# Kernel tuning notes

Hardware: AMD Instinct MI355X
Metric: run time of the kernel (lower is better)

The kernel has to match this reference:

```python
import jax, jax.numpy as jnp
import numpy as np

N = 100000   # nodes
E = 1600000  # edges
G = 256      # graphs in batch
F_IN = 64
H = 64
C = 10


def setup_inputs() -> dict:
    key = jax.random.key(0)
    ks = jax.random.split(key, 16)
    x = jax.random.normal(ks[0], (N, F_IN), dtype=jnp.float32)
    edge_index = jax.random.randint(ks[1], (2, E), 0, N, dtype=jnp.int32)
    batch = jnp.sort(jax.random.randint(ks[2], (N,), 0, G, dtype=jnp.int32))
    def lin(k, i, o):
        return jax.random.normal(k, (i, o), dtype=jnp.float32) / np.sqrt(i).astype(np.float32)
    return {
        'x': x, 'edge_index': edge_index, 'batch': batch,
        'W1': lin(ks[3], F_IN, H), 'b1': jnp.zeros((H,), jnp.float32),
        'W2': lin(ks[4], H, H),    'b2': jnp.zeros((H,), jnp.float32),
        'W3': lin(ks[5], H, H),    'b3': jnp.zeros((H,), jnp.float32),
        'fc1_w': lin(ks[6], 3 * H, H),      'fc1_b': jnp.zeros((H,), jnp.float32),
        'fc2_w': lin(ks[7], H, H // 2),     'fc2_b': jnp.zeros((H // 2,), jnp.float32),
        'fc3_w': lin(ks[8], H // 2, C),     'fc3_b': jnp.zeros((C,), jnp.float32),
    }


def _gcn_layer(h_in, W, b, src, dst, deg_inv_sqrt):
    # GCNConv: h = X W ; out = D^-1/2 (A + I) D^-1/2 h + b ; then ReLU
    h = h_in @ W
    norm = deg_inv_sqrt[src] * deg_inv_sqrt[dst]            # [E]
    agg = jax.ops.segment_sum(h[src] * norm[:, None], dst, num_segments=N)
    agg = agg + h * (deg_inv_sqrt * deg_inv_sqrt)[:, None]  # self-loop term
    return jax.nn.relu(agg + b)


def _pool(h, batch):
    # concat(mean, max, add) pooling by graph id
    s = jax.ops.segment_sum(h, batch, num_segments=G)
    cnt = jax.ops.segment_sum(jnp.ones((h.shape[0], 1), h.dtype), batch, num_segments=G)
    mean = s / jnp.maximum(cnt, 1.0)
    mx = jnp.maximum(jax.ops.segment_max(h, batch, num_segments=G), 0.0)  # h >= 0 post-ReLU
    return jnp.concatenate([mean, mx, s], axis=1)  # [G, 3H]


def reference(x, edge_index, batch, W1, b1, W2, b2, W3, b3,
              fc1_w, fc1_b, fc2_w, fc2_b, fc3_w, fc3_b):
    src, dst = edge_index[0], edge_index[1]
    # degree including self loop (edge weight 1)
    deg = jax.ops.segment_sum(jnp.ones((E,), x.dtype), dst, num_segments=N) + 1.0
    dis = jax.lax.rsqrt(deg)

    h1 = _gcn_layer(x, W1, b1, src, dst, dis)
    p1 = _pool(h1, batch)
    h2 = _gcn_layer(h1, W2, b2, src, dst, dis)
    p2 = _pool(h2, batch)
    h3 = _gcn_layer(h2, W3, b3, src, dst, dis)
    p3 = _pool(h3, batch)

    z = p1 + p2 + p3                              # [G, 3H]
    z = jax.nn.relu(z @ fc1_w + fc1_b)            # dropout inactive (eval)
    z = jax.nn.relu(z @ fc2_w + fc2_b)
    return jax.nn.log_softmax(z @ fc3_w + fc3_b, axis=-1)
```

## Files before the change

kernel.cpp:

```cpp
#include <hip/hip_runtime.h>
#include <cmath>

typedef unsigned int uint;
typedef __attribute__((ext_vector_type(8))) short short8;
typedef __attribute__((ext_vector_type(4))) float f32x4;
typedef __attribute__((ext_vector_type(4))) int i32x4;

__device__ inline float bflo(uint u) { return __uint_as_float(u << 16); }
__device__ inline float bfhi(uint u) { return __uint_as_float(u & 0xffff0000u); }
__device__ inline ushort bf1(float a) {
  uint ua = __float_as_uint(a);
  return (ushort)((ua + 0x7fffu + ((ua >> 16) & 1u)) >> 16);
}
__device__ inline uint bfpack(float a, float b) {
  uint ua = __float_as_uint(a), ub = __float_as_uint(b);
  uint ra = (ua + 0x7fffu + ((ua >> 16) & 1u)) >> 16;
  uint rb = (ub + 0x7fffu + ((ub >> 16) & 1u)) >> 16;
  return ra | (rb << 16);
}

#define SLOT_CAP 48
#define FILL_CHUNK 4096
#define BSHIFT 8
#define NPB 256
#define MAXB 512
#define BCAP 5120

__global__ __launch_bounds__(256) void part_k(const int* __restrict__ src, const int* __restrict__ dst,
                                              int* __restrict__ bcnt, long long* __restrict__ buckets,
                                              int E, int nb) {
  __shared__ int lcnt[MAXB], lbase[MAXB];
  int t = threadIdx.x;
  for (int i = t; i < nb; i += 256) lcnt[i] = 0;
  __syncthreads();
  int base = blockIdx.x * FILL_CHUNK;
  int d[16];
  #pragma unroll
  for (int i = 0; i < 16; ++i) {
    int e = base + t + i * 256;
    d[i] = (e < E) ? __builtin_nontemporal_load(dst + e) : -1;
    if (d[i] >= 0) atomicAdd(&lcnt[d[i] >> BSHIFT], 1);
  }
  __syncthreads();
  for (int i = t; i < nb; i += 256) { lbase[i] = atomicAdd(&bcnt[i], lcnt[i]); lcnt[i] = 0; }
  __syncthreads();
  #pragma unroll
  for (int i = 0; i < 16; ++i) {
    if (d[i] >= 0) {
      int e = base + t + i * 256;
      int r = d[i] >> BSHIFT;
      int rank = atomicAdd(&lcnt[r], 1);
      long long s = (long long)__builtin_nontemporal_load(src + e);
      long long packed = (s << 32) | (unsigned int)d[i];
      buckets[(size_t)r * BCAP + lbase[r] + rank] = packed;
    }
  }
}

__global__ __launch_bounds__(256) void fillB_k(const long long* __restrict__ buckets,
                                               const int* __restrict__ bcnt,
                                               int* __restrict__ cursor, int* __restrict__ csr,
                                               int nb, int N) {
  __shared__ int lcnt[NPB];
  __shared__ int rows[NPB][SLOT_CAP];
  int r = blockIdx.x;
  int t = threadIdx.x;
  if (t < NPB) lcnt[t] = 0;
  i32x4* rinit = (i32x4*)&rows[0][0];
  for (int i = t; i < NPB * SLOT_CAP / 4; i += 256) rinit[i] = (i32x4){N, N, N, N};
  __syncthreads();
  int n = bcnt[r];
  const long long* bk = buckets + (size_t)r * BCAP;
  for (int i = t; i < n; i += 256) {
    long long e = __builtin_nontemporal_load(&bk[i]);
    int dl = (int)(e & (NPB - 1));
    int s = (int)(e >> 32);
    int pos = atomicAdd(&lcnt[dl], 1);
    if (pos < SLOT_CAP) rows[dl][pos] = s;
  }
  __syncthreads();
  int base_node = r << BSHIFT;
  int nodes_here = N - base_node; if (nodes_here > NPB) nodes_here = NPB;
  if (nodes_here <= 0) return;
  int total4 = nodes_here * (SLOT_CAP / 4);
  i32x4* dstp = (i32x4*)(csr + (size_t)base_node * SLOT_CAP);
  const i32x4* srcp = (const i32x4*)&rows[0][0];
  for (int i = t; i < total4; i += 256) dstp[i] = srcp[i];
  for (int i = t; i < nodes_here; i += 256) cursor[base_node + i] = lcnt[i];
}

__global__ __launch_bounds__(256) void dis_k(const int* __restrict__ cursor, float* __restrict__ dis, int n) {
  int i = blockIdx.x * 256 + threadIdx.x;
  if (i < n) dis[i] = rsqrtf((float)cursor[i] + 1.0f);
}

__global__ __launch_bounds__(256) void bounds_k(const int* __restrict__ batch, int* __restrict__ gstart,
                                                int n, int G) {
  int i = blockIdx.x * 256 + threadIdx.x;
  if (i >= n) return;
  int b = batch[i];
  int prev = (i == 0) ? -1 : batch[i - 1];
  for (int g = prev + 1; g <= b; ++g) gstart[g] = i;
  if (i == n - 1) { for (int g = b + 1; g <= G; ++g) gstart[g] = n; }
}

__global__ __launch_bounds__(256) void xcast_k(const float* __restrict__ X, ushort* __restrict__ Y, int total4) {
  int i = blockIdx.x * 256 + threadIdx.x;
  if (i >= total4) return;
  float4 v = ((const float4*)X)[i];
  ((uint2*)Y)[i] = make_uint2(bfpack(v.x, v.y), bfpack(v.z, v.w));
}

__global__ __launch_bounds__(256) void wt_k(const float* __restrict__ W, ushort* __restrict__ WT) {
  int i = blockIdx.x * 256 + threadIdx.x;
  int c = i >> 6, k = i & 63;
  WT[i] = bf1(W[k * 64 + c]);
}

__global__ __launch_bounds__(256) void gemm_mfma_k(const ushort* __restrict__ X,
                                                   const ushort* __restrict__ WT,
                                                   const float* __restrict__ dis,
                                                   ushort* __restrict__ Y, int n) {
  int t = threadIdx.x;
  int wv = t >> 6, lane = t & 63;
  int m = lane & 15, quad = lane >> 4;
  int row = blockIdx.x * 64 + wv * 16 + m;
  int rclamp = (row < n) ? row : 0;
  const short8* arow = (const short8*)(X + (size_t)rclamp * 64);
  short8 a0 = arow[quad];
  short8 a1 = arow[quad + 4];
  f32x4 acc[4];
  #pragma unroll
  for (int ct = 0; ct < 4; ++ct) {
    const short8* wrow = (const short8*)(WT + (size_t)(ct * 16 + m) * 64);
    short8 b0 = wrow[quad];
    short8 b1 = wrow[quad + 4];
    f32x4 a = {0.f, 0.f, 0.f, 0.f};
    a = __builtin_amdgcn_mfma_f32_16x16x32_bf16(a0, b0, a, 0, 0, 0);
    a = __builtin_amdgcn_mfma_f32_16x16x32_bf16(a1, b1, a, 0, 0, 0);
    acc[ct] = a;
  }
  int orow = blockIdx.x * 64 + wv * 16 + quad * 4;
  #pragma unroll
  for (int reg = 0; reg < 4; ++reg) {
    int r = orow + reg;
    if (r < n) {
      float ds = dis[r];
      #pragma unroll
      for (int ct = 0; ct < 4; ++ct)
        Y[(size_t)r * 64 + ct * 16 + m] = bf1(acc[ct][reg] * ds);
    }
  }
}

__global__ __launch_bounds__(256) void agg_k(const ushort* __restrict__ Hs,
                                             const int* __restrict__ csr,
                                             const int* __restrict__ cnt,
                                             const float* __restrict__ dis,
                                             const float* __restrict__ bias,
                                             ushort* __restrict__ Hout, int n) {
  int wv = __builtin_amdgcn_readfirstlane((int)(threadIdx.x >> 6));
  int lane = threadIdx.x & 63;
  int node = blockIdx.x * 4 + wv;
  if (node >= n) return;
  float dn = dis[node];
  int deg = __builtin_nontemporal_load(cnt + node);
  if (deg > SLOT_CAP) deg = SLOT_CAP;
  const i32x4* rp = (const i32x4*)(csr + (size_t)node * SLOT_CAP);
  float acc = bflo((uint)Hs[(size_t)node * 64 + lane]);

  i32x4 ra0 = __builtin_nontemporal_load(rp + 0);
  i32x4 ra1 = __builtin_nontemporal_load(rp + 1);
  i32x4 ra2 = __builtin_nontemporal_load(rp + 2);
  i32x4 ra3 = __builtin_nontemporal_load(rp + 3);
  int sa[16] = {ra0.x, ra0.y, ra0.z, ra0.w,
                ra1.x, ra1.y, ra1.z, ra1.w,
                ra2.x, ra2.y, ra2.z, ra2.w,
                ra3.x, ra3.y, ra3.z, ra3.w};
  float ha[16];
  #pragma unroll
  for (int i = 0; i < 16; ++i) ha[i] = bflo((uint)Hs[(size_t)sa[i] * 64 + lane]);
  #pragma unroll
  for (int i = 0; i < 16; ++i) acc += ha[i];

  if (deg > 16) {
    i32x4 rb0 = __builtin_nontemporal_load(rp + 4);
    i32x4 rb1 = __builtin_nontemporal_load(rp + 5);
    i32x4 rb2 = __builtin_nontemporal_load(rp + 6);
    i32x4 rb3 = __builtin_nontemporal_load(rp + 7);
    int sb[16] = {rb0.x, rb0.y, rb0.z, rb0.w,
                  rb1.x, rb1.y, rb1.z, rb1.w,
                  rb2.x, rb2.y, rb2.z, rb2.w,
                  rb3.x, rb3.y, rb3.z, rb3.w};
    float hb[16];
    #pragma unroll
    for (int i = 0; i < 16; ++i) hb[i] = bflo((uint)Hs[(size_t)sb[i] * 64 + lane]);
    #pragma unroll
    for (int i = 0; i < 16; ++i) acc += hb[i];

    if (deg > 32) {
      i32x4 rc0 = __builtin_nontemporal_load(rp + 8);
      i32x4 rc1 = __builtin_nontemporal_load(rp + 9);
      i32x4 rc2 = __builtin_nontemporal_load(rp + 10);
      i32x4 rc3 = __builtin_nontemporal_load(rp + 11);
      int sc[16] = {rc0.x, rc0.y, rc0.z, rc0.w,
                    rc1.x, rc1.y, rc1.z, rc1.w,
                    rc2.x, rc2.y, rc2.z, rc2.w,
                    rc3.x, rc3.y, rc3.z, rc3.w};
      float hc[16];
      #pragma unroll
      for (int i = 0; i < 16; ++i) hc[i] = bflo((uint)Hs[(size_t)sc[i] * 64 + lane]);
      #pragma unroll
      for (int i = 0; i < 16; ++i) acc += hc[i];
    }
  }

  float v = fmaxf(fmaf(dn, acc, bias[lane]), 0.f);
  Hout[(size_t)node * 64 + lane] = bf1(v);
}

__global__ __launch_bounds__(256) void pool_k(const ushort* __restrict__ H, const int* __restrict__ gstart,
                                              float* __restrict__ z) {
  int g = blockIdx.x;
  int t = threadIdx.x;
  int lane = t & 63, w = t >> 6;
  int slot = lane >> 3, fl = lane & 7;
  int i0 = gstart[g], i1 = gstart[g + 1];
  float s[8], m[8];
  #pragma unroll
  for (int j = 0; j < 8; ++j) { s[j] = 0.f; m[j] = 0.f; }
  for (int i = i0 + w * 8 + slot; i < i1; i += 32) {
    uint4 v = ((const uint4*)(H + (size_t)i * 64))[fl];
    float f[8] = { bflo(v.x), bfhi(v.x), bflo(v.y), bfhi(v.y),
                   bflo(v.z), bfhi(v.z), bflo(v.w), bfhi(v.w) };
    #pragma unroll
    for (int j = 0; j < 8; ++j) { s[j] += f[j]; m[j] = fmaxf(m[j], f[j]); }
  }
  #pragma unroll
  for (int msk = 8; msk <= 32; msk <<= 1) {
    #pragma unroll
    for (int j = 0; j < 8; ++j) {
      s[j] += __shfl_xor(s[j], msk, 64);
      m[j] = fmaxf(m[j], __shfl_xor(m[j], msk, 64));
    }
  }
  __shared__ float ss[4][64], sm[4][64];
  if (slot == 0) {
    #pragma unroll
    for (int j = 0; j < 8; ++j) { ss[w][fl * 8 + j] = s[j]; sm[w][fl * 8 + j] = m[j]; }
  }
  __syncthreads();
  if (t < 64) {
    float S = ss[0][t] + ss[1][t] + ss[2][t] + ss[3][t];
    float M = fmaxf(fmaxf(sm[0][t], sm[1][t]), fmaxf(sm[2][t], sm[3][t]));
    float cnt = (float)(i1 - i0);
    float mean = (cnt > 0.f) ? S / cnt : 0.f;
    z[g * 192 + t]       += mean;
    z[g * 192 + 64 + t]  += M;
    z[g * 192 + 128 + t] += S;
  }
}

__global__ __launch_bounds__(64) void mlp_k(const float* __restrict__ z,
                                            const float* __restrict__ fc1w, const float* __restrict__ fc1b,
                                            const float* __restrict__ fc2w, const float* __restrict__ fc2b,
                                            const float* __restrict__ fc3w, const float* __restrict__ fc3b,
                                            float* __restrict__ out) {
  int g = blockIdx.x; int t = threadIdx.x;
  __shared__ float zr[192], a1[64], a2[32], a3[10];
  for (int i = t; i < 192; i += 64) zr[i] = z[g * 192 + i];
  __syncthreads();
  float acc = fc1b[t];
  for (int k = 0; k < 192; ++k) acc += zr[k] * fc1w[k * 64 + t];
  a1[t] = fmaxf(acc, 0.f);
  __syncthreads();
  if (t < 32) {
    float a = fc2b[t];
    #pragma unroll
    for (int k = 0; k < 64; ++k) a += a1[k] * fc2w[k * 32 + t];
    a2[t] = fmaxf(a, 0.f);
  }
  __syncthreads();
  if (t < 10) {
    float a = fc3b[t];
    #pragma unroll
    for (int k = 0; k < 32; ++k) a += a2[k] * fc3w[k * 10 + t];
    a3[t] = a;
  }
  __syncthreads();
  if (t == 0) {
    float mx = a3[0];
    for (int i = 1; i < 10; ++i) mx = fmaxf(mx, a3[i]);
    float sum = 0.f;
    for (int i = 0; i < 10; ++i) sum += expf(a3[i] - mx);
    float lse = mx + logf(sum);
    for (int i = 0; i < 10; ++i) out[g * 10 + i] = a3[i] - lse;
  }
}

extern "C" void kernel_launch(void* const* d_in, const int* in_sizes, int n_in,
                              void* d_out, int out_size, void* d_ws, size_t ws_size,
                              hipStream_t stream) {
  const float* x    = (const float*)d_in[0];
  const int*   ei   = (const int*)  d_in[1];
  const int*   batch= (const int*)  d_in[2];
  const float* W1   = (const float*)d_in[3];
  const float* b1   = (const float*)d_in[4];
  const float* W2   = (const float*)d_in[5];
  const float* b2   = (const float*)d_in[6];
  const float* W3   = (const float*)d_in[7];
  const float* b3   = (const float*)d_in[8];
  const float* fc1w = (const float*)d_in[9];
  const float* fc1b = (const float*)d_in[10];
  const float* fc2w = (const float*)d_in[11];
  const float* fc2b = (const float*)d_in[12];
  const float* fc3w = (const float*)d_in[13];
  const float* fc3b = (const float*)d_in[14];
  float* out = (float*)d_out;

  const int N = in_sizes[0] / 64;
  const int E = in_sizes[1] / 2;
  const int G = out_size / 10;
  const int* src = ei;
  const int* dst = ei + E;
  const int nb = (N + NPB - 1) >> BSHIFT;

  char* p = (char*)d_ws;
  auto alloc = [&](size_t bytes) -> void* {
    void* r = (void*)p; p += (bytes + 255) & ~(size_t)255; return r;
  };
  int*       cursor  = (int*)      alloc((size_t)N * 4);
  int*       bcnt    = (int*)      alloc(MAXB * 4);
  float*     dis     = (float*)    alloc((size_t)N * 4);
  int*       gstart  = (int*)      alloc((size_t)(G + 1) * 4);
  int*       csr     = (int*)      alloc((size_t)(nb * NPB) * SLOT_CAP * 4);
  long long* buckets = (long long*)alloc((size_t)nb * BCAP * 8);
  ushort*    xbf     = (ushort*)   alloc((size_t)N * 64 * 2);
  ushort*    wt1     = (ushort*)   alloc(4096 * 2);
  ushort*    wt2     = (ushort*)   alloc(4096 * 2);
  ushort*    wt3     = (ushort*)   alloc(4096 * 2);
  ushort*    hlin    = (ushort*)   alloc((size_t)(N + 1) * 64 * 2);
  ushort*    hA      = (ushort*)   alloc((size_t)N * 64 * 2);
  float*     zbuf    = (float*)    alloc((size_t)G * 192 * 4);
  (void)ws_size; (void)n_in;

  (void)hipMemsetAsync(bcnt, 0, MAXB * 4, stream);
  (void)hipMemsetAsync(zbuf, 0, (size_t)G * 192 * 4, stream);
  (void)hipMemsetAsync(hlin + (size_t)N * 64, 0, 64 * 2, stream);

  int chunks = (E + FILL_CHUNK - 1) / FILL_CHUNK;
  part_k<<<chunks, 256, 0, stream>>>(src, dst, bcnt, buckets, E, nb);
  fillB_k<<<nb, 256, 0, stream>>>(buckets, bcnt, cursor, csr, nb, N);
  dis_k<<<(N + 255) / 256, 256, 0, stream>>>(cursor, dis, N);
  bounds_k<<<(N + 255) / 256, 256, 0, stream>>>(batch, gstart, N, G);
  xcast_k<<<(N * 16 + 255) / 256, 256, 0, stream>>>(x, xbf, N * 16);
  wt_k<<<16, 256, 0, stream>>>(W1, wt1);
  wt_k<<<16, 256, 0, stream>>>(W2, wt2);
  wt_k<<<16, 256, 0, stream>>>(W3, wt3);

  int gb = (N + 63) / 64;
  int ab = (N + 3) / 4;
  gemm_mfma_k<<<gb, 256, 0, stream>>>(xbf, wt1, dis, hlin, N);
  agg_k<<<ab, 256, 0, stream>>>(hlin, csr, cursor, dis, b1, hA, N);
  pool_k<<<G, 256, 0, stream>>>(hA, gstart, zbuf);
  gemm_mfma_k<<<gb, 256, 0, stream>>>(hA, wt2, dis, hlin, N);
  agg_k<<<ab, 256, 0, stream>>>(hlin, csr, cursor, dis, b2, hA, N);
  pool_k<<<G, 256, 0, stream>>>(hA, gstart, zbuf);
  gemm_mfma_k<<<gb, 256, 0, stream>>>(hA, wt3, dis, hlin, N);
  agg_k<<<ab, 256, 0, stream>>>(hlin, csr, cursor, dis, b3, hA, N);
  pool_k<<<G, 256, 0, stream>>>(hA, gstart, zbuf);

  mlp_k<<<G, 64, 0, stream>>>(zbuf, fc1w, fc1b, fc2w, fc2b, fc3w, fc3b, out);
}
```

Before: 332.8 us.

## Fuse dis into fillB, merge weight casts, split pooling, widen agg first batch

Folds the degree-to-rsqrt computation into the CSR fill kernel and merges the three weight-transpose launches into one, removing small kernel launches. The pooling kernel is split four ways per graph, accumulating partial sums and maxima with atomics, and the mean/concat step moves into the MLP kernel. The aggregation kernel now unconditionally gathers 32 neighbours up front instead of 16, trading extra padded-slot loads for fewer branches and more memory-level parallelism. Float atomic adds make the summation order nondeterministic.

```diff
diff --git a/kernel.cpp b/kernel.cpp
--- a/kernel.cpp
+++ b/kernel.cpp
@@ -25,6 +25,7 @@
 #define NPB 256
 #define MAXB 512
 #define BCAP 5120
+#define PSPLIT 4
 
 __global__ __launch_bounds__(256) void part_k(const int* __restrict__ src, const int* __restrict__ dst,
                                               int* __restrict__ bcnt, long long* __restrict__ buckets,
@@ -60,6 +61,7 @@
 __global__ __launch_bounds__(256) void fillB_k(const long long* __restrict__ buckets,
                                                const int* __restrict__ bcnt,
                                                int* __restrict__ cursor, int* __restrict__ csr,
+                                               float* __restrict__ dis,
                                                int nb, int N) {
   __shared__ int lcnt[NPB];
   __shared__ int rows[NPB][SLOT_CAP];
@@ -86,12 +88,11 @@
   i32x4* dstp = (i32x4*)(csr + (size_t)base_node * SLOT_CAP);
   const i32x4* srcp = (const i32x4*)&rows[0][0];
   for (int i = t; i < total4; i += 256) dstp[i] = srcp[i];
-  for (int i = t; i < nodes_here; i += 256) cursor[base_node + i] = lcnt[i];
-}
-
-__global__ __launch_bounds__(256) void dis_k(const int* __restrict__ cursor, float* __restrict__ dis, int n) {
-  int i = blockIdx.x * 256 + threadIdx.x;
-  if (i < n) dis[i] = rsqrtf((float)cursor[i] + 1.0f);
+  for (int i = t; i < nodes_here; i += 256) {
+    int c = lcnt[i];
+    cursor[base_node + i] = c;
+    dis[base_node + i] = rsqrtf((float)c + 1.0f);
+  }
 }
 
 __global__ __launch_bounds__(256) void bounds_k(const int* __restrict__ batch, int* __restrict__ gstart,
@@ -111,10 +112,16 @@
   ((uint2*)Y)[i] = make_uint2(bfpack(v.x, v.y), bfpack(v.z, v.w));
 }
 
-__global__ __launch_bounds__(256) void wt_k(const float* __restrict__ W, ushort* __restrict__ WT) {
-  int i = blockIdx.x * 256 + threadIdx.x;
+__global__ __launch_bounds__(256) void wt3_k(const float* __restrict__ W1, const float* __restrict__ W2,
+                                             const float* __restrict__ W3,
+                                             ushort* __restrict__ T1, ushort* __restrict__ T2,
+                                             ushort* __restrict__ T3) {
+  int b = blockIdx.x >> 4;
+  int i = (blockIdx.x & 15) * 256 + threadIdx.x;
+  const float* W = (b == 0) ? W1 : (b == 1) ? W2 : W3;
+  ushort* T = (b == 0) ? T1 : (b == 1) ? T2 : T3;
   int c = i >> 6, k = i & 63;
-  WT[i] = bf1(W[k * 64 + c]);
+  T[i] = bf1(W[k * 64 + c]);
 }
 
 __global__ __launch_bounds__(256) void gemm_mfma_k(const ushort* __restrict__ X,
@@ -169,50 +176,36 @@
   const i32x4* rp = (const i32x4*)(csr + (size_t)node * SLOT_CAP);
   float acc = bflo((uint)Hs[(size_t)node * 64 + lane]);
 
-  i32x4 ra0 = __builtin_nontemporal_load(rp + 0);
-  i32x4 ra1 = __builtin_nontemporal_load(rp + 1);
-  i32x4 ra2 = __builtin_nontemporal_load(rp + 2);
-  i32x4 ra3 = __builtin_nontemporal_load(rp + 3);
-  int sa[16] = {ra0.x, ra0.y, ra0.z, ra0.w,
-                ra1.x, ra1.y, ra1.z, ra1.w,
-                ra2.x, ra2.y, ra2.z, ra2.w,
-                ra3.x, ra3.y, ra3.z, ra3.w};
-  float ha[16];
-  #pragma unroll
-  for (int i = 0; i < 16; ++i) ha[i] = bflo((uint)Hs[(size_t)sa[i] * 64 + lane]);
-  #pragma unroll
-  for (int i = 0; i < 16; ++i) acc += ha[i];
-
-  if (deg > 16) {
-    i32x4 rb0 = __builtin_nontemporal_load(rp + 4);
-    i32x4 rb1 = __builtin_nontemporal_load(rp + 5);
-    i32x4 rb2 = __builtin_nontemporal_load(rp + 6);
-    i32x4 rb3 = __builtin_nontemporal_load(rp + 7);
-    int sb[16] = {rb0.x, rb0.y, rb0.z, rb0.w,
-                  rb1.x, rb1.y, rb1.z, rb1.w,
-                  rb2.x, rb2.y, rb2.z, rb2.w,
-                  rb3.x, rb3.y, rb3.z, rb3.w};
+  i32x4 r0 = __builtin_nontemporal_load(rp + 0);
+  i32x4 r1 = __builtin_nontemporal_load(rp + 1);
+  i32x4 r2 = __builtin_nontemporal_load(rp + 2);
+  i32x4 r3 = __builtin_nontemporal_load(rp + 3);
+  i32x4 r4 = __builtin_nontemporal_load(rp + 4);
+  i32x4 r5 = __builtin_nontemporal_load(rp + 5);
+  i32x4 r6 = __builtin_nontemporal_load(rp + 6);
+  i32x4 r7 = __builtin_nontemporal_load(rp + 7);
+  int sa[32] = {r0.x, r0.y, r0.z, r0.w, r1.x, r1.y, r1.z, r1.w,
+                r2.x, r2.y, r2.z, r2.w, r3.x, r3.y, r3.z, r3.w,
+                r4.x, r4.y, r4.z, r4.w, r5.x, r5.y, r5.z, r5.w,
+                r6.x, r6.y, r6.z, r6.w, r7.x, r7.y, r7.z, r7.w};
+  float ha[32];
+  #pragma unroll
+  for (int i = 0; i < 32; ++i) ha[i] = bflo((uint)Hs[(size_t)sa[i] * 64 + lane]);
+  #pragma unroll
+  for (int i = 0; i < 32; ++i) acc += ha[i];
+
+  if (deg > 32) {
+    i32x4 r8  = __builtin_nontemporal_load(rp + 8);
+    i32x4 r9  = __builtin_nontemporal_load(rp + 9);
+    i32x4 r10 = __builtin_nontemporal_load(rp + 10);
+    i32x4 r11 = __builtin_nontemporal_load(rp + 11);
+    int sb[16] = {r8.x, r8.y, r8.z, r8.w, r9.x, r9.y, r9.z, r9.w,
+                  r10.x, r10.y, r10.z, r10.w, r11.x, r11.y, r11.z, r11.w};
     float hb[16];
     #pragma unroll
     for (int i = 0; i < 16; ++i) hb[i] = bflo((uint)Hs[(size_t)sb[i] * 64 + lane]);
     #pragma unroll
     for (int i = 0; i < 16; ++i) acc += hb[i];
-
-    if (deg > 32) {
-      i32x4 rc0 = __builtin_nontemporal_load(rp + 8);
-      i32x4 rc1 = __builtin_nontemporal_load(rp + 9);
-      i32x4 rc2 = __builtin_nontemporal_load(rp + 10);
-      i32x4 rc3 = __builtin_nontemporal_load(rp + 11);
-      int sc[16] = {rc0.x, rc0.y, rc0.z, rc0.w,
-                    rc1.x, rc1.y, rc1.z, rc1.w,
-                    rc2.x, rc2.y, rc2.z, rc2.w,
-                    rc3.x, rc3.y, rc3.z, rc3.w};
-      float hc[16];
-      #pragma unroll
-      for (int i = 0; i < 16; ++i) hc[i] = bflo((uint)Hs[(size_t)sc[i] * 64 + lane]);
-      #pragma unroll
-      for (int i = 0; i < 16; ++i) acc += hc[i];
-    }
   }
 
   float v = fmaxf(fmaf(dn, acc, bias[lane]), 0.f);
@@ -220,8 +213,9 @@
 }
 
 __global__ __launch_bounds__(256) void pool_k(const ushort* __restrict__ H, const int* __restrict__ gstart,
-                                              float* __restrict__ z) {
-  int g = blockIdx.x;
+                                              float* __restrict__ zsum, uint* __restrict__ zmax) {
+  int g = blockIdx.x / PSPLIT;
+  int q = blockIdx.x % PSPLIT;
   int t = threadIdx.x;
   int lane = t & 63, w = t >> 6;
   int slot = lane >> 3, fl = lane & 7;
@@ -229,7 +223,7 @@
   float s[8], m[8];
   #pragma unroll
   for (int j = 0; j < 8; ++j) { s[j] = 0.f; m[j] = 0.f; }
-  for (int i = i0 + w * 8 + slot; i < i1; i += 32) {
+  for (int i = i0 + q * 32 + w * 8 + slot; i < i1; i += 32 * PSPLIT) {
     uint4 v = ((const uint4*)(H + (size_t)i * 64))[fl];
     float f[8] = { bflo(v.x), bfhi(v.x), bflo(v.y), bfhi(v.y),
                    bflo(v.z), bfhi(v.z), bflo(v.w), bfhi(v.w) };
@@ -251,24 +245,30 @@
   }
   __syncthreads();
   if (t < 64) {
-    float S = ss[0][t] + ss[1][t] + ss[2][t] + ss[3][t];
+    float S = (ss[0][t] + ss[1][t]) + (ss[2][t] + ss[3][t]);
     float M = fmaxf(fmaxf(sm[0][t], sm[1][t]), fmaxf(sm[2][t], sm[3][t]));
-    float cnt = (float)(i1 - i0);
-    float mean = (cnt > 0.f) ? S / cnt : 0.f;
-    z[g * 192 + t]       += mean;
-    z[g * 192 + 64 + t]  += M;
-    z[g * 192 + 128 + t] += S;
-  }
-}
-
-__global__ __launch_bounds__(64) void mlp_k(const float* __restrict__ z,
+    atomicAdd(&zsum[g * 64 + t], S);
+    atomicMax(&zmax[g * 64 + t], __float_as_uint(M));
+  }
+}
+
+__global__ __launch_bounds__(64) void mlp_k(const float* __restrict__ zsum,
+                                            const uint* __restrict__ zmax, int G64,
+                                            const int* __restrict__ gstart,
                                             const float* __restrict__ fc1w, const float* __restrict__ fc1b,
                                             const float* __restrict__ fc2w, const float* __restrict__ fc2b,
                                             const float* __restrict__ fc3w, const float* __restrict__ fc3b,
                                             float* __restrict__ out) {
   int g = blockIdx.x; int t = threadIdx.x;
   __shared__ float zr[192], a1[64], a2[32], a3[10];
-  for (int i = t; i < 192; i += 64) zr[i] = z[g * 192 + i];
+  float S = zsum[g * 64 + t];
+  float M = __uint_as_float(zmax[g * 64 + t])
+          + __uint_as_float(zmax[G64 + g * 64 + t])
+          + __uint_as_float(zmax[2 * G64 + g * 64 + t]);
+  float cntf = (float)(gstart[g + 1] - gstart[g]);
+  zr[t]       = (cntf > 0.f) ? S / cntf : 0.f;
+  zr[64 + t]  = M;
+  zr[128 + t] = S;
   __syncthreads();
   float acc = fc1b[t];
   for (int k = 0; k < 192; ++k) acc += zr[k] * fc1w[k * 64 + t];
@@ -341,34 +341,34 @@
   ushort*    wt3     = (ushort*)   alloc(4096 * 2);
   ushort*    hlin    = (ushort*)   alloc((size_t)(N + 1) * 64 * 2);
   ushort*    hA      = (ushort*)   alloc((size_t)N * 64 * 2);
-  float*     zbuf    = (float*)    alloc((size_t)G * 192 * 4);
+  float*     zsum    = (float*)    alloc((size_t)G * 64 * 4);
+  uint*      zmax    = (uint*)     alloc((size_t)3 * G * 64 * 4);
   (void)ws_size; (void)n_in;
 
   (void)hipMemsetAsync(bcnt, 0, MAXB * 4, stream);
-  (void)hipMemsetAsync(zbuf, 0, (size_t)G * 192 * 4, stream);
+  (void)hipMemsetAsync(zsum, 0, (size_t)G * 64 * 4, stream);
+  (void)hipMemsetAsync(zmax, 0, (size_t)3 * G * 64 * 4, stream);
   (void)hipMemsetAsync(hlin + (size_t)N * 64, 0, 64 * 2, stream);
 
   int chunks = (E + FILL_CHUNK - 1) / FILL_CHUNK;
   part_k<<<chunks, 256, 0, stream>>>(src, dst, bcnt, buckets, E, nb);
-  fillB_k<<<nb, 256, 0, stream>>>(buckets, bcnt, cursor, csr, nb, N);
-  dis_k<<<(N + 255) / 256, 256, 0, stream>>>(cursor, dis, N);
+  fillB_k<<<nb, 256, 0, stream>>>(buckets, bcnt, cursor, csr, dis, nb, N);
   bounds_k<<<(N + 255) / 256, 256, 0, stream>>>(batch, gstart, N, G);
   xcast_k<<<(N * 16 + 255) / 256, 256, 0, stream>>>(x, xbf, N * 16);
-  wt_k<<<16, 256, 0, stream>>>(W1, wt1);
-  wt_k<<<16, 256, 0, stream>>>(W2, wt2);
-  wt_k<<<16, 256, 0, stream>>>(W3, wt3);
+  wt3_k<<<48, 256, 0, stream>>>(W1, W2, W3, wt1, wt2, wt3);
 
   int gb = (N + 63) / 64;
   int ab = (N + 3) / 4;
+  int G64 = G * 64;
   gemm_mfma_k<<<gb, 256, 0, stream>>>(xbf, wt1, dis, hlin, N);
   agg_k<<<ab, 256, 0, stream>>>(hlin, csr, cursor, dis, b1, hA, N);
-  pool_k<<<G, 256, 0, stream>>>(hA, gstart, zbuf);
+  pool_k<<<G * PSPLIT, 256, 0, stream>>>(hA, gstart, zsum, zmax + 0 * G64);
   gemm_mfma_k<<<gb, 256, 0, stream>>>(hA, wt2, dis, hlin, N);
   agg_k<<<ab, 256, 0, stream>>>(hlin, csr, cursor, dis, b2, hA, N);
-  pool_k<<<G, 256, 0, stream>>>(hA, gstart, zbuf);
+  pool_k<<<G * PSPLIT, 256, 0, stream>>>(hA, gstart, zsum, zmax + 1 * G64);
   gemm_mfma_k<<<gb, 256, 0, stream>>>(hA, wt3, dis, hlin, N);
   agg_k<<<ab, 256, 0, stream>>>(hlin, csr, cursor, dis, b3, hA, N);
-  pool_k<<<G, 256, 0, stream>>>(hA, gstart, zbuf);
-
-  mlp_k<<<G, 64, 0, stream>>>(zbuf, fc1w, fc1b, fc2w, fc2b, fc3w, fc3b, out);
-}
+  pool_k<<<G * PSPLIT, 256, 0, stream>>>(hA, gstart, zsum, zmax + 2 * G64);
+
+  mlp_k<<<G, 64, 0, stream>>>(zsum, zmax, G64, gstart, fc1w, fc1b, fc2w, fc2b, fc3w, fc3b, out);
+}
```

Result: faster. 321.1 us (-3.5%).
